# Optimization experiments

Measured on AMD Instinct MI355X. Metric: run time of the kernel, lower is better.

Reference implementation:

```python
import jax, jax.numpy as jnp
import numpy as np

B, V, P, D = 32, 6, 197, 512
L = 77          # CLIP token length
C = 5           # num quality perspectives (conditions)

def _normalize(x, axis=-1, eps=1e-12):
    n = jnp.linalg.norm(x, axis=axis, keepdims=True)
    return x / jnp.maximum(n, eps)

def _conv3x3(x, w, b):
    # x: [C,112,7,7], w: [O,112,3,3] -> [C,O,7,7]
    y = jax.lax.conv_general_dilated(x, w, (1, 1), 'SAME',
                                     dimension_numbers=('NCHW', 'OIHW', 'NCHW'))
    return y + b[None, :, None, None]

def setup_inputs() -> dict:
    key = jax.random.key(0)
    ks = jax.random.split(key, 20)
    s = 0.02  # weight init scale keeps sigmoids in linear-ish range
    return {
        'feature_texture': jax.random.normal(ks[0], (B, V * P, D), jnp.float32),
        'feature_prompt': jax.random.normal(ks[1], (B, L, D), jnp.float32),
        'feature_prompt_eot': jax.random.normal(ks[2], (B, D), jnp.float32),
        'feature_condition': jax.random.normal(ks[3], (C, D), jnp.float32),
        'fc_quality_w': jax.random.normal(ks[4], (224, D), jnp.float32) * s,
        'fc_quality_b': jnp.zeros((224,), jnp.float32),
        'fc_condition_w': jax.random.normal(ks[5], (5488, D), jnp.float32) * s,
        'fc_condition_b': jnp.zeros((5488,), jnp.float32),
        'fc1w_conv_w': jax.random.normal(ks[6], (512, 112, 3, 3), jnp.float32) * s,
        'fc1w_conv_b': jnp.zeros((512,), jnp.float32),
        'fc2w_conv_w': jax.random.normal(ks[7], (128, 112, 3, 3), jnp.float32) * s,
        'fc2w_conv_b': jnp.zeros((128,), jnp.float32),
        'fc3w_conv_w': jax.random.normal(ks[8], (32, 112, 3, 3), jnp.float32) * s,
        'fc3w_conv_b': jnp.zeros((32,), jnp.float32),
        'fc4w_conv_w': jax.random.normal(ks[9], (8, 112, 3, 3), jnp.float32) * s,
        'fc4w_conv_b': jnp.zeros((8,), jnp.float32),
        'fc1b_w': jax.random.normal(ks[10], (112, 112), jnp.float32) * s,
        'fc1b_b': jnp.zeros((112,), jnp.float32),
        'fc2b_w': jax.random.normal(ks[11], (56, 112), jnp.float32) * s,
        'fc2b_b': jnp.zeros((56,), jnp.float32),
        'fc3b_w': jax.random.normal(ks[12], (28, 112), jnp.float32) * s,
        'fc3b_b': jnp.zeros((28,), jnp.float32),
        'fc4b_w': jax.random.normal(ks[13], (14, 112), jnp.float32) * s,
        'fc4b_b': jnp.zeros((14,), jnp.float32),
        'fc5w_w': jax.random.normal(ks[14], (14, 112), jnp.float32) * s,
        'fc5w_b': jnp.zeros((14,), jnp.float32),
        'fc5b_w': jax.random.normal(ks[15], (1, 112), jnp.float32) * s,
        'fc5b_b': jnp.zeros((1,), jnp.float32),
    }

def reference(feature_texture, feature_prompt, feature_prompt_eot, feature_condition,
              fc_quality_w, fc_quality_b, fc_condition_w, fc_condition_b,
              fc1w_conv_w, fc1w_conv_b, fc2w_conv_w, fc2w_conv_b,
              fc3w_conv_w, fc3w_conv_b, fc4w_conv_w, fc4w_conv_b,
              fc1b_w, fc1b_b, fc2b_w, fc2b_b, fc3b_w, fc3b_b, fc4b_w, fc4b_b,
              fc5w_w, fc5w_b, fc5b_w, fc5b_b):
    nC = feature_condition.shape[0]

    # --- calculate_cos: mean of relu(pairwise cosine sim), upper triangle i<j ---
    fn = _normalize(feature_condition)                      # [C,512]
    gram = fn @ fn.T                                        # [C,C]
    iu, ju = jnp.triu_indices(nC, k=1)
    loss_dis = jnp.mean(jnp.maximum(gram[iu, ju], 0.0))

    # --- cross-attention-style patch weighting ---
    np_prompt = _normalize(feature_prompt, axis=2)          # [B,L,D]
    np_tex = _normalize(feature_texture, axis=2)            # [B,J,D]
    sim_texture = jnp.einsum('bid,bjd->bji', np_prompt, np_tex)   # [B,J,L]
    sim_cond = jnp.einsum('bid,cd->bci', np_prompt, fn)           # [B,C,L]
    patch_weight = jnp.einsum('bcl,bjl->bjc', sim_cond, sim_texture)  # [B,J,C]
    patch_weight = jax.nn.softmax(patch_weight, axis=1)

    # --- condition feature maps for hypernet: [C,112,7,7] ---
    cond_maps = (feature_condition @ fc_condition_w.T + fc_condition_b)
    cond_maps = cond_maps.reshape(nC, 112, 7, 7)

    # --- hypernet: generate TargetNet params for all conditions at once ---
    pooled = cond_maps.mean(axis=(2, 3))                              # [C,112]
    fc1w = _conv3x3(cond_maps, fc1w_conv_w, fc1w_conv_b).reshape(nC, 112, 224)
    fc2w = _conv3x3(cond_maps, fc2w_conv_w, fc2w_conv_b).reshape(nC, 56, 112)
    fc3w = _conv3x3(cond_maps, fc3w_conv_w, fc3w_conv_b).reshape(nC, 28, 56)
    fc4w = _conv3x3(cond_maps, fc4w_conv_w, fc4w_conv_b).reshape(nC, 14, 28)
    fc1b = pooled @ fc1b_w.T + fc1b_b                                 # [C,112]
    fc2b = pooled @ fc2b_w.T + fc2b_b                                 # [C,56]
    fc3b = pooled @ fc3b_w.T + fc3b_b                                 # [C,28]
    fc4b = pooled @ fc4b_w.T + fc4b_b                                 # [C,14]
    fc5w = pooled @ fc5w_w.T + fc5w_b                                 # [C,14]
    fc5b = pooled @ fc5b_w.T + fc5b_b                                 # [C,1]

    # --- fused quality feature per (batch, condition) ---
    ftf = jnp.einsum('bjd,bjc->bcd', feature_texture, patch_weight)   # [B,C,D]
    fused = ftf * feature_prompt_eot[:, None, :]                      # [B,C,D]
    fq = jnp.einsum('bcd,kd->bck', fused, fc_quality_w) + fc_quality_b  # [B,C,224]

    # --- TargetNet (per-condition generated weights), vectorized over loop ---
    h = jax.nn.sigmoid(jnp.einsum('bck,cjk->bcj', fq, fc1w) + fc1b[None])
    h = jax.nn.sigmoid(jnp.einsum('bcj,cij->bci', h, fc2w) + fc2b[None])
    h = jax.nn.sigmoid(jnp.einsum('bci,coi->bco', h, fc3w) + fc3b[None])
    h = jax.nn.sigmoid(jnp.einsum('bco,cpo->bcp', h, fc4w) + fc4b[None])
    score_list = jnp.einsum('bcp,cp->bc', h, fc5w) + fc5b[:, 0][None]  # [B,C]

    return score_list, loss_dis
```

## Files before the change

### kernel.cpp

```cpp
#include <hip/hip_runtime.h>
#include <hip/hip_bf16.h>
#include <math.h>

#define B_   32
#define J_   1182
#define D_   512
#define L_   77
#define C_   5
#define JC_  64
#define NCH_ 19
#define NPW_ 37

__device__ __forceinline__ float dot4(float4 a, float4 b) {
    return a.x*b.x + a.y*b.y + a.z*b.z + a.w*b.w;
}

__device__ __forceinline__ float wave_sum(float v) {
#pragma unroll
    for (int off = 32; off > 0; off >>= 1) v += __shfl_xor(v, off, 64);
    return v;
}

__device__ __forceinline__ float wave_max(float v) {
#pragma unroll
    for (int off = 32; off > 0; off >>= 1) v = fmaxf(v, __shfl_xor(v, off, 64));
    return v;
}

__global__ void k_front(const float* __restrict__ fc, const float* __restrict__ cw,
                        const float* __restrict__ cb, float* __restrict__ cm,
                        float* __restrict__ loss_out,
                        const float* __restrict__ fp, float* __restrict__ swl) {
    __shared__ float4 smem4[640];
    float* sfc = (float*)smem4;
    int bid = blockIdx.x, t = threadIdx.x;
    int wave = t >> 6, lane = t & 63;

    if (bid < 1373) {
        for (int i = t; i < C_*D_; i += 256) sfc[i] = fc[i];
        __syncthreads();

        if (bid == 1372) {
            for (int c = wave; c < C_; c += 4) {
                float ss = 0.f;
                for (int d = lane; d < D_; d += 64) { float v = sfc[c*D_+d]; ss += v*v; }
                ss = wave_sum(ss);
                float inv = 1.f / fmaxf(sqrtf(ss), 1e-12f);
                for (int d = lane; d < D_; d += 64) sfc[c*D_+d] *= inv;
            }
            __syncthreads();
            if (wave == 0) {
                float acc = 0.f;
                for (int i = 0; i < C_; ++i)
                    for (int j = i+1; j < C_; ++j) {
                        float p = 0.f;
                        for (int d = lane; d < D_; d += 64) p += sfc[i*D_+d]*sfc[j*D_+d];
                        p = wave_sum(p);
                        acc += fmaxf(p, 0.f);
                    }
                if (lane == 0) *loss_out = acc * (1.f/10.f);
            }
            return;
        }

        int o = bid*4 + wave;
        const float4* w4 = (const float4*)(cw + (size_t)o*D_);
        float4 wa = w4[lane], wb = w4[lane+64];
        float bias = cb[o];
        float keep = 0.f;
#pragma unroll
        for (int c = 0; c < C_; ++c) {
            const float4* f4 = (const float4*)(sfc + c*D_);
            float s = dot4(wa, f4[lane]) + dot4(wb, f4[lane+64]);
            s = wave_sum(s);
            if (lane == c) keep = s;
        }
        if (lane < C_) cm[lane*5488 + o] = keep + bias;
        return;
    }

    for (int c = wave; c < C_; c += 4) {
        const float4* f8 = (const float4*)(fc + c*D_);
        float4 v0 = f8[lane*2], v1 = f8[lane*2+1];
        float ss = dot4(v0,v0) + dot4(v1,v1);
        ss = wave_sum(ss);
        float inv = 1.f / fmaxf(sqrtf(ss), 1e-12f);
        v0.x*=inv; v0.y*=inv; v0.z*=inv; v0.w*=inv;
        v1.x*=inv; v1.y*=inv; v1.z*=inv; v1.w*=inv;
        int f0 = lane*2, f1 = lane*2+1;
        smem4[(c*16 + (f0 & 15))*8 + (f0 >> 4)] = v0;
        smem4[(c*16 + (f1 & 15))*8 + (f1 >> 4)] = v1;
    }
    __syncthreads();

    int row = t >> 3, seg = t & 7;
    int bl = (bid - 1373)*32 + row;
    int b = bl / L_, l = bl - b*L_;
    const float4* p4 = ((const float4*)(fp + (size_t)bl*D_)) + seg*16;
    float ss=0.f, s0=0.f, s1=0.f, s2=0.f, s3=0.f, s4=0.f;
#pragma unroll 4
    for (int k = 0; k < 16; ++k) {
        float4 v = p4[k];
        int base = k*8 + seg;
        ss += dot4(v, v);
        s0 += dot4(v, smem4[base]);
        s1 += dot4(v, smem4[128 + base]);
        s2 += dot4(v, smem4[256 + base]);
        s3 += dot4(v, smem4[384 + base]);
        s4 += dot4(v, smem4[512 + base]);
    }
#pragma unroll
    for (int off = 1; off < 8; off <<= 1) {
        ss += __shfl_xor(ss,off,64);
        s0 += __shfl_xor(s0,off,64); s1 += __shfl_xor(s1,off,64);
        s2 += __shfl_xor(s2,off,64); s3 += __shfl_xor(s3,off,64);
        s4 += __shfl_xor(s4,off,64);
    }
    if (seg == 0) {
        float inv = 1.f / fmaxf(sqrtf(ss), 1e-12f);
        float inv2 = inv*inv;
        swl[((size_t)(b*C_+0))*L_ + l] = s0*inv2;
        swl[((size_t)(b*C_+1))*L_ + l] = s1*inv2;
        swl[((size_t)(b*C_+2))*L_ + l] = s2*inv2;
        swl[((size_t)(b*C_+3))*L_ + l] = s3*inv2;
        swl[((size_t)(b*C_+4))*L_ + l] = s4*inv2;
    }
}

__global__ void k_Q(const float* __restrict__ fp, const float* __restrict__ swl,
                    float* __restrict__ Q) {
    __shared__ float sw[C_][80];
    int b = blockIdx.y;
    int t = threadIdx.x;
    for (int i = t; i < C_*L_; i += 256) { int c = i/L_, l = i - c*L_; sw[c][l] = swl[((size_t)(b*C_+c))*L_ + l]; }
    __syncthreads();
    int d = blockIdx.x*256 + t;
    float a0=0.f, a1=0.f, a2=0.f, a3=0.f, a4=0.f;
    const float* f = fp + (size_t)b*L_*D_ + d;
    for (int l = 0; l < L_; ++l) {
        float v = f[(size_t)l*D_];
        a0 += sw[0][l]*v; a1 += sw[1][l]*v; a2 += sw[2][l]*v;
        a3 += sw[3][l]*v; a4 += sw[4][l]*v;
    }
    Q[(size_t)(b*C_+0)*D_ + d] = a0;
    Q[(size_t)(b*C_+1)*D_ + d] = a1;
    Q[(size_t)(b*C_+2)*D_ + d] = a2;
    Q[(size_t)(b*C_+3)*D_ + d] = a3;
    Q[(size_t)(b*C_+4)*D_ + d] = a4;
}

__global__ void k_conv_pw(const float* __restrict__ cm,
                          const float* __restrict__ w1, const float* __restrict__ bb1,
                          const float* __restrict__ w2, const float* __restrict__ bb2,
                          const float* __restrict__ w3, const float* __restrict__ bb3,
                          const float* __restrict__ w4, const float* __restrict__ bb4,
                          float* __restrict__ o1, float* __restrict__ o2,
                          float* __restrict__ o3, float* __restrict__ o4,
                          const float* __restrict__ w1b, const float* __restrict__ b1b,
                          const float* __restrict__ w2b, const float* __restrict__ b2b,
                          const float* __restrict__ w3b, const float* __restrict__ b3b,
                          const float* __restrict__ w4b, const float* __restrict__ b4b,
                          const float* __restrict__ w5w, const float* __restrict__ b5w,
                          const float* __restrict__ w5b, const float* __restrict__ b5b,
                          float* __restrict__ fcb,
                          const float* __restrict__ tex, const float* __restrict__ Q,
                          float* __restrict__ pw, float2* __restrict__ pstat) {
    __shared__ float4 smem4[3052];
    __shared__ float sp[112];
    int bid = blockIdx.x;
    int t = threadIdx.x;
    bool is_conv = (bid < 1500) && ((bid & 3) == 0);

    if (!is_conv) {
        int p = (bid >= 1500) ? (bid - 375) : (bid - 1 - (bid >> 2));
        float4* qs = smem4;
        float* sraw = (float*)(smem4 + 640);
        int bx = p % NPW_, b = p / NPW_;
        {
            const float4* q4 = (const float4*)(Q + (size_t)b*C_*D_);
            for (int i = t; i < C_*128; i += 256) {
                int c = i >> 7, f = i & 127;
                qs[(c*16 + (f & 15))*8 + (f >> 4)] = q4[i];
            }
        }
        __syncthreads();
        int row = t >> 3, seg = t & 7;
        int j = bx*32 + row;
        bool valid = (j < J_);
        int jc = valid ? j : (J_-1);
        const float4* tp = (const float4*)(tex + ((size_t)(b*J_ + jc))*D_ + seg*64);
        float ss=0.f, s0=0.f, s1=0.f, s2=0.f, s3=0.f, s4=0.f;
#pragma unroll 4
        for (int k = 0; k < 16; ++k) {
            float4 v = tp[k];
            int base = k*8 + seg;
            ss += dot4(v, v);
            s0 += dot4(v, qs[base]);
            s1 += dot4(v, qs[128 + base]);
            s2 += dot4(v, qs[256 + base]);
            s3 += dot4(v, qs[384 + base]);
            s4 += dot4(v, qs[512 + base]);
        }
#pragma unroll
        for (int off = 1; off < 8; off <<= 1) {
            ss += __shfl_xor(ss,off,64);
            s0 += __shfl_xor(s0,off,64); s1 += __shfl_xor(s1,off,64);
            s2 += __shfl_xor(s2,off,64); s3 += __shfl_xor(s3,off,64);
            s4 += __shfl_xor(s4,off,64);
        }
        if (seg == 0) {
            float inv = 1.f / fmaxf(sqrtf(ss), 1e-12f);
            float r0 = s0*inv, r1 = s1*inv, r2 = s2*inv, r3 = s3*inv, r4 = s4*inv;
            if (valid) {
                pw[((size_t)(b*C_+0))*J_ + j] = r0;
                pw[((size_t)(b*C_+1))*J_ + j] = r1;
                pw[((size_t)(b*C_+2))*J_ + j] = r2;
                pw[((size_t)(b*C_+3))*J_ + j] = r3;
                pw[((size_t)(b*C_+4))*J_ + j] = r4;
                sraw[0*32+row]=r0; sraw[1*32+row]=r1; sraw[2*32+row]=r2;
                sraw[3*32+row]=r3; sraw[4*32+row]=r4;
            } else {
                sraw[0*32+row]=-1e30f; sraw[1*32+row]=-1e30f; sraw[2*32+row]=-1e30f;
                sraw[3*32+row]=-1e30f; sraw[4*32+row]=-1e30f;
            }
        }
        __syncthreads();
        if (t < C_*32) {
            int c = t >> 5, r2 = t & 31;
            float v = sraw[c*32 + r2];
            float m = v;
#pragma unroll
            for (int off = 1; off < 32; off <<= 1) m = fmaxf(m, __shfl_xor(m,off,32));
            float e = (v > -1e29f) ? expf(v - m) : 0.f;
#pragma unroll
            for (int off = 1; off < 32; off <<= 1) e += __shfl_xor(e,off,32);
            if (r2 == 0) pstat[(size_t)(bx*B_ + b)*C_ + c] = make_float2(m, e);
        }
        return;
    }

    int conv_id = bid >> 2;
    float* im = (float*)smem4;
    int c  = conv_id / 75;
    int bx = conv_id - c*75;
    for (int i = t; i < 112*108; i += 256) im[i] = 0.f;
    __syncthreads();
    const float* cmc = cm + c*5488;
    for (int i = t; i < 112*49; i += 256) {
        int ch = i / 49, yx = i - ch*49;
        int y = yx / 7, x = yx - y*7;
        im[ch*108 + (y+1)*12 + (x+1)] = cmc[i];
    }
    __syncthreads();

    if (bx == 0) {
        if (t < 112) {
            const float* p = im + t*108;
            float s = 0.f;
            for (int k = 0; k < 108; ++k) s += p[k];
            sp[t] = s * (1.f/49.f);
        }
        __syncthreads();
        if (t < 225) {
            int rel = t;
            const float* w; const float* bb; int nout; int base;
            if      (rel < 112) {            w=w1b; bb=b1b; nout=112; base=0; }
            else if (rel < 168) { rel-=112;  w=w2b; bb=b2b; nout=56;  base=560; }
            else if (rel < 196) { rel-=168;  w=w3b; bb=b3b; nout=28;  base=840; }
            else if (rel < 210) { rel-=196;  w=w4b; bb=b4b; nout=14;  base=980; }
            else if (rel < 224) { rel-=210;  w=w5w; bb=b5w; nout=14;  base=1050; }
            else                { rel-=224;  w=w5b; bb=b5b; nout=1;   base=1120; }
            float s = bb[rel];
            const float* wr = w + rel*112;
            for (int i = 0; i < 112; ++i) s += sp[i]*wr[i];
            fcb[base + c*nout + rel] = s;
        }
    }

    int oyl = t & 63;
    int chq = t >> 6;
    int oy  = bx*64 + oyl;
    bool ovalid = (oy < 4760);
    int oyc = ovalid ? oy : 0;
    int o_comb = oyc / 7, y = oyc - o_comb*7;
    const float* w; int o;
    if      (o_comb < 512) { w=w1; o=o_comb; }
    else if (o_comb < 640) { w=w2; o=o_comb-512; }
    else if (o_comb < 672) { w=w3; o=o_comb-640; }
    else                   { w=w4; o=o_comb-672; }

    float ac0=0,ac1=0,ac2=0,ac3=0,ac4=0,ac5=0,ac6=0;
    const float* wbase = w + ((size_t)o*112 + chq*28)*9;
    const float* imc   = im + (chq*28)*108 + y*12;
#pragma unroll 2
    for (int ch = 0; ch < 28; ++ch) {
        const float* wk = wbase + ch*9;
        const float* ii = imc + ch*108;
        float w0=wk[0],w1_=wk[1],w2_=wk[2],w3_=wk[3],w4_=wk[4],w5_=wk[5],w6_=wk[6],w7_=wk[7],w8_=wk[8];
#pragma unroll
        for (int ky = 0; ky < 3; ++ky) {
            const float* row = ii + ky*12;
            float4 ra = *(const float4*)(row);
            float4 rb = *(const float4*)(row + 4);
            float  rc = row[8];
            float r0=ra.x,r1=ra.y,r2=ra.z,r3=ra.w,r4=rb.x,r5=rb.y,r6=rb.z,r7=rb.w,r8=rc;
            float wk0 = (ky==0)?w0:((ky==1)?w3_:w6_);
            float wk1 = (ky==0)?w1_:((ky==1)?w4_:w7_);
            float wk2 = (ky==0)?w2_:((ky==1)?w5_:w8_);
            ac0 += r0*wk0 + r1*wk1 + r2*wk2;
            ac1 += r1*wk0 + r2*wk1 + r3*wk2;
            ac2 += r2*wk0 + r3*wk1 + r4*wk2;
            ac3 += r3*wk0 + r4*wk1 + r5*wk2;
            ac4 += r4*wk0 + r5*wk1 + r6*wk2;
            ac5 += r5*wk0 + r6*wk1 + r7*wk2;
            ac6 += r6*wk0 + r7*wk1 + r8*wk2;
        }
    }
    __syncthreads();
    float* partb = im;
    {
        int pb = (chq*64 + oyl)*9;
        partb[pb+0]=ac0; partb[pb+1]=ac1; partb[pb+2]=ac2; partb[pb+3]=ac3;
        partb[pb+4]=ac4; partb[pb+5]=ac5; partb[pb+6]=ac6;
    }
    __syncthreads();
    for (int i = t; i < 448; i += 256) {
        int oyl2 = i / 7, x = i - oyl2*7;
        int oy2 = bx*64 + oyl2;
        if (oy2 < 4760) {
            float s = partb[(0*64+oyl2)*9+x] + partb[(1*64+oyl2)*9+x]
                    + partb[(2*64+oyl2)*9+x] + partb[(3*64+oyl2)*9+x];
            int oc = oy2/7, yy = oy2 - oc*7;
            const float* bias; float* outp; int oo;
            if      (oc < 512) { bias=bb1; outp=o1 + (size_t)c*512*49; oo=oc; }
            else if (oc < 640) { bias=bb2; outp=o2 + (size_t)c*128*49; oo=oc-512; }
            else if (oc < 672) { bias=bb3; outp=o3 + (size_t)c*32*49;  oo=oc-640; }
            else               { bias=bb4; outp=o4 + (size_t)c*8*49;   oo=oc-672; }
            outp[oo*49 + yy*7 + x] = s + bias[oo];
        }
    }
}

__global__ void k_ftf(const float* __restrict__ tex, const float* __restrict__ pwraw,
                      const float2* __restrict__ pstat, float* __restrict__ part) {
    __shared__ float sw[C_][JC_];
    __shared__ float2 sL[C_];
    int chunk = blockIdx.x, b = blockIdx.y;
    int t = threadIdx.x;
    int wave = t >> 6, lane = t & 63;
    if (wave < C_) {
        float2 pv = (lane < NPW_) ? pstat[(size_t)(lane*B_ + b)*C_ + wave]
                                  : make_float2(-1e30f, 0.f);
        float m = wave_max(pv.x);
        float contrib = (lane < NPW_) ? pv.y * expf(pv.x - m) : 0.f;
        float denom = wave_sum(contrib);
        if (lane == 0) sL[wave] = make_float2(m, 1.f/denom);
    }
    __syncthreads();
    int j0 = chunk*JC_;
    int jn = min(JC_, J_ - j0);
    if (t < C_*JC_) {
        int c = t >> 6, jj = t & 63;
        float2 ms = sL[c];
        sw[c][jj] = (jj < jn)
            ? expf(pwraw[((size_t)(b*C_+c))*J_ + j0 + jj] - ms.x) * ms.y
            : 0.f;
    }
    __syncthreads();
    float acc0=0.f, acc1=0.f, acc2=0.f, acc3=0.f, acc4=0.f;
    const float* tp = tex + ((size_t)b*J_ + j0)*D_ + t;
    for (int jj = 0; jj < jn; ++jj) {
        float v = tp[(size_t)jj*D_];
        acc0 += v*sw[0][jj]; acc1 += v*sw[1][jj]; acc2 += v*sw[2][jj];
        acc3 += v*sw[3][jj]; acc4 += v*sw[4][jj];
    }
    size_t base = (((size_t)chunk*B_ + b)*C_)*D_ + t;
    part[base               ] = acc0;
    part[base +   (size_t)D_] = acc1;
    part[base + 2*(size_t)D_] = acc2;
    part[base + 3*(size_t)D_] = acc3;
    part[base + 4*(size_t)D_] = acc4;
}

__global__ void k_fq_target(const float* __restrict__ part, const float* __restrict__ eot,
                            const float* __restrict__ qw, const float* __restrict__ qb,
                            const float* __restrict__ g1w, const float* __restrict__ g2w,
                            const float* __restrict__ g3w, const float* __restrict__ g4w,
                            const float* __restrict__ fcb, float* __restrict__ out) {
    int bc = blockIdx.x; int b = bc / C_; int c = bc - b*C_;
    __shared__ float sf[D_];
    __shared__ float sa[224], sb[112];
    int t = threadIdx.x;

    float s0 = 0.f, s1 = 0.f;
    for (int ch = 0; ch < NCH_; ++ch) {
        const float* p = part + ((size_t)ch*(B_*C_) + bc)*D_;
        s0 += p[t]; s1 += p[t+256];
    }
    sf[t]     = s0 * eot[b*D_ + t];
    sf[t+256] = s1 * eot[b*D_ + t + 256];
    __syncthreads();

    if (t < 224) {
        const float4* w4 = (const float4*)(qw + (size_t)t*D_);
        const float4* s4 = (const float4*)sf;
        float acc = 0.f;
#pragma unroll 4
        for (int i = 0; i < 128; ++i) acc += dot4(s4[i], w4[i]);
        sa[t] = acc + qb[t];
    }
    __syncthreads();

    if (t < 112) {
        const float* w = g1w + (size_t)c*25088 + t*224;
        float s = fcb[c*112 + t];
        for (int k = 0; k < 224; ++k) s += w[k]*sa[k];
        sb[t] = 1.f/(1.f+expf(-s));
    }
    __syncthreads();
    if (t < 56) {
        const float* w = g2w + (size_t)c*6272 + t*112;
        float s = fcb[560 + c*56 + t];
        for (int k = 0; k < 112; ++k) s += w[k]*sb[k];
        sa[t] = 1.f/(1.f+expf(-s));
    }
    __syncthreads();
    if (t < 28) {
        const float* w = g3w + (size_t)c*1568 + t*56;
        float s = fcb[840 + c*28 + t];
        for (int k = 0; k < 56; ++k) s += w[k]*sa[k];
        sb[t] = 1.f/(1.f+expf(-s));
    }
    __syncthreads();
    if (t < 14) {
        const float* w = g4w + (size_t)c*392 + t*28;
        float s = fcb[980 + c*14 + t];
        for (int k = 0; k < 28; ++k) s += w[k]*sb[k];
        sa[t] = 1.f/(1.f+expf(-s));
    }
    __syncthreads();
    if (t == 0) {
        float s = fcb[1120 + c];
        for (int p = 0; p < 14; ++p) s += sa[p]*fcb[1050 + c*14 + p];
        out[b*C_ + c] = s;
    }
}

extern "C" void kernel_launch(void* const* d_in, const int* in_sizes, int n_in,
                              void* d_out, int out_size, void* d_ws, size_t ws_size,
                              hipStream_t stream) {
    (void)in_sizes; (void)n_in; (void)out_size; (void)ws_size;
    const float* tex   = (const float*)d_in[0];
    const float* fp    = (const float*)d_in[1];
    const float* eot   = (const float*)d_in[2];
    const float* fcond = (const float*)d_in[3];
    const float* qw    = (const float*)d_in[4];
    const float* qb    = (const float*)d_in[5];
    const float* cw    = (const float*)d_in[6];
    const float* cb    = (const float*)d_in[7];
    const float* w1c   = (const float*)d_in[8];  const float* b1c = (const float*)d_in[9];
    const float* w2c   = (const float*)d_in[10]; const float* b2c = (const float*)d_in[11];
    const float* w3c   = (const float*)d_in[12]; const float* b3c = (const float*)d_in[13];
    const float* w4c   = (const float*)d_in[14]; const float* b4c = (const float*)d_in[15];
    const float* f1bw  = (const float*)d_in[16]; const float* f1bb = (const float*)d_in[17];
    const float* f2bw  = (const float*)d_in[18]; const float* f2bb = (const float*)d_in[19];
    const float* f3bw  = (const float*)d_in[20]; const float* f3bb = (const float*)d_in[21];
    const float* f4bw  = (const float*)d_in[22]; const float* f4bb = (const float*)d_in[23];
    const float* f5ww  = (const float*)d_in[24]; const float* f5wb = (const float*)d_in[25];
    const float* f5bw  = (const float*)d_in[26]; const float* f5bb = (const float*)d_in[27];
    float* out = (float*)d_out;

    float* ws     = (float*)d_ws;
    float* Qb     = ws;
    float* pw     = Qb + 81920;
    float* part   = pw + 189120;
    float* pstat  = part + 1556480;
    float* cm     = pstat + 11840;
    float* g1w    = cm + 27440;
    float* g2w    = g1w + 125440;
    float* g3w    = g2w + 31360;
    float* g4w    = g3w + 7840;
    float* fcb    = g4w + 1960;
    float* swl    = fcb + 1125;

    k_front<<<1450, 256, 0, stream>>>(fcond, cw, cb, cm, out + B_*C_, fp, swl);
    k_Q<<<dim3(2, B_), 256, 0, stream>>>(fp, swl, Qb);
    k_conv_pw<<<1559, 256, 0, stream>>>(cm, w1c, b1c, w2c, b2c, w3c, b3c, w4c, b4c,
                                        g1w, g2w, g3w, g4w,
                                        f1bw, f1bb, f2bw, f2bb, f3bw, f3bb,
                                        f4bw, f4bb, f5ww, f5wb, f5bw, f5bb, fcb,
                                        tex, Qb, pw, (float2*)pstat);
    k_ftf<<<dim3(NCH_, B_), 512, 0, stream>>>(tex, pw, (const float2*)pstat, part);
    k_fq_target<<<B_*C_, 256, 0, stream>>>(part, eot, qw, qb,
                                           g1w, g2w, g3w, g4w, fcb, out);
}
```

Before: 101.7 us.

## Stage texture rows in padded LDS and shrink patch-weight tiles to 16 rows

The patch-weight part of the fused conv kernel now loads 16 texture rows per block with coalesced float4 reads into padded shared memory, then computes norms and query dot products from LDS with 16 lanes per row. Previously each block handled 32 rows read directly from global memory. The conv blocks are no longer interleaved with the patch-weight blocks; they occupy the first 375 block IDs. Doubling the number of patch-weight tiles doubles the partial softmax stats, so the k_ftf reduction reads two stats per lane and the workspace offsets are shifted. This adds occupancy pressure from roughly 48KB of LDS per block in exchange for better load coalescing and more parallelism.

```diff
diff --git a/kernel.cpp b/kernel.cpp
--- a/kernel.cpp
+++ b/kernel.cpp
@@ -9,7 +9,8 @@
 #define C_   5
 #define JC_  64
 #define NCH_ 19
-#define NPW_ 37
+#define NPW_ 74
+#define JPW_ 16
 
 __device__ __forceinline__ float dot4(float4 a, float4 b) {
     return a.x*b.x + a.y*b.y + a.z*b.z + a.w*b.w;
@@ -165,84 +166,103 @@
                           float* __restrict__ fcb,
                           const float* __restrict__ tex, const float* __restrict__ Q,
                           float* __restrict__ pw, float2* __restrict__ pstat) {
-    __shared__ float4 smem4[3052];
-    __shared__ float sp[112];
+    __shared__ float smem[12352];
     int bid = blockIdx.x;
     int t = threadIdx.x;
-    bool is_conv = (bid < 1500) && ((bid & 3) == 0);
-
-    if (!is_conv) {
-        int p = (bid >= 1500) ? (bid - 375) : (bid - 1 - (bid >> 2));
-        float4* qs = smem4;
-        float* sraw = (float*)(smem4 + 640);
+
+    if (bid >= 375) {
+        float* stex = smem;
+        float* sq   = smem + 9216;
+        float* srawT = smem + 12096;
+        int p = bid - 375;
         int bx = p % NPW_, b = p / NPW_;
+        int j0 = bx*JPW_;
+        int jn = min(JPW_, J_ - j0);
+
         {
             const float4* q4 = (const float4*)(Q + (size_t)b*C_*D_);
             for (int i = t; i < C_*128; i += 256) {
-                int c = i >> 7, f = i & 127;
-                qs[(c*16 + (f & 15))*8 + (f >> 4)] = q4[i];
+                int c = i >> 7, col4 = i & 127;
+                *(float4*)(sq + c*576 + col4*4 + ((col4>>3)<<2)) = q4[i];
+            }
+            const float4* t4 = (const float4*)(tex + ((size_t)(b*J_ + j0))*D_);
+#pragma unroll
+            for (int n = 0; n < 8; ++n) {
+                int i = n*256 + t;
+                int row = i >> 7, col4 = i & 127;
+                if (row < jn)
+                    *(float4*)(stex + row*576 + col4*4 + ((col4>>3)<<2)) = t4[i];
             }
         }
         __syncthreads();
-        int row = t >> 3, seg = t & 7;
-        int j = bx*32 + row;
-        bool valid = (j < J_);
-        int jc = valid ? j : (J_-1);
-        const float4* tp = (const float4*)(tex + ((size_t)(b*J_ + jc))*D_ + seg*64);
-        float ss=0.f, s0=0.f, s1=0.f, s2=0.f, s3=0.f, s4=0.f;
-#pragma unroll 4
-        for (int k = 0; k < 16; ++k) {
-            float4 v = tp[k];
-            int base = k*8 + seg;
-            ss += dot4(v, v);
-            s0 += dot4(v, qs[base]);
-            s1 += dot4(v, qs[128 + base]);
-            s2 += dot4(v, qs[256 + base]);
-            s3 += dot4(v, qs[384 + base]);
-            s4 += dot4(v, qs[512 + base]);
-        }
-#pragma unroll
-        for (int off = 1; off < 8; off <<= 1) {
-            ss += __shfl_xor(ss,off,64);
-            s0 += __shfl_xor(s0,off,64); s1 += __shfl_xor(s1,off,64);
-            s2 += __shfl_xor(s2,off,64); s3 += __shfl_xor(s3,off,64);
-            s4 += __shfl_xor(s4,off,64);
-        }
-        if (seg == 0) {
-            float inv = 1.f / fmaxf(sqrtf(ss), 1e-12f);
-            float r0 = s0*inv, r1 = s1*inv, r2 = s2*inv, r3 = s3*inv, r4 = s4*inv;
-            if (valid) {
-                pw[((size_t)(b*C_+0))*J_ + j] = r0;
-                pw[((size_t)(b*C_+1))*J_ + j] = r1;
-                pw[((size_t)(b*C_+2))*J_ + j] = r2;
-                pw[((size_t)(b*C_+3))*J_ + j] = r3;
-                pw[((size_t)(b*C_+4))*J_ + j] = r4;
-                sraw[0*32+row]=r0; sraw[1*32+row]=r1; sraw[2*32+row]=r2;
-                sraw[3*32+row]=r3; sraw[4*32+row]=r4;
-            } else {
-                sraw[0*32+row]=-1e30f; sraw[1*32+row]=-1e30f; sraw[2*32+row]=-1e30f;
-                sraw[3*32+row]=-1e30f; sraw[4*32+row]=-1e30f;
+
+        {
+            int row = t >> 4, seg = t & 15;
+            const float* sr = stex + row*576;
+            float ss=0.f, s0=0.f, s1=0.f, s2=0.f, s3=0.f, s4=0.f;
+#pragma unroll
+            for (int k = 0; k < 8; ++k) {
+                int col4 = seg*8 + k;
+                int wa = col4*4 + ((col4>>3)<<2);
+                float4 v = *(const float4*)(sr + wa);
+                ss += dot4(v, v);
+                s0 += dot4(v, *(const float4*)(sq +          wa));
+                s1 += dot4(v, *(const float4*)(sq +   576 + wa));
+                s2 += dot4(v, *(const float4*)(sq + 2*576 + wa));
+                s3 += dot4(v, *(const float4*)(sq + 3*576 + wa));
+                s4 += dot4(v, *(const float4*)(sq + 4*576 + wa));
+            }
+#pragma unroll
+            for (int off = 1; off < 16; off <<= 1) {
+                ss += __shfl_xor(ss,off,64);
+                s0 += __shfl_xor(s0,off,64); s1 += __shfl_xor(s1,off,64);
+                s2 += __shfl_xor(s2,off,64); s3 += __shfl_xor(s3,off,64);
+                s4 += __shfl_xor(s4,off,64);
+            }
+            if (seg == 0) {
+                if (row < jn) {
+                    float inv = 1.f / fmaxf(sqrtf(ss), 1e-12f);
+                    float r0=s0*inv, r1=s1*inv, r2=s2*inv, r3=s3*inv, r4=s4*inv;
+                    int j = j0 + row;
+                    pw[((size_t)(b*C_+0))*J_ + j] = r0;
+                    pw[((size_t)(b*C_+1))*J_ + j] = r1;
+                    pw[((size_t)(b*C_+2))*J_ + j] = r2;
+                    pw[((size_t)(b*C_+3))*J_ + j] = r3;
+                    pw[((size_t)(b*C_+4))*J_ + j] = r4;
+                    srawT[row*8+0]=r0; srawT[row*8+1]=r1; srawT[row*8+2]=r2;
+                    srawT[row*8+3]=r3; srawT[row*8+4]=r4;
+                } else {
+                    srawT[row*8+0]=-1e30f; srawT[row*8+1]=-1e30f; srawT[row*8+2]=-1e30f;
+                    srawT[row*8+3]=-1e30f; srawT[row*8+4]=-1e30f;
+                }
             }
         }
         __syncthreads();
-        if (t < C_*32) {
-            int c = t >> 5, r2 = t & 31;
-            float v = sraw[c*32 + r2];
-            float m = v;
-#pragma unroll
-            for (int off = 1; off < 32; off <<= 1) m = fmaxf(m, __shfl_xor(m,off,32));
-            float e = (v > -1e29f) ? expf(v - m) : 0.f;
-#pragma unroll
-            for (int off = 1; off < 32; off <<= 1) e += __shfl_xor(e,off,32);
-            if (r2 == 0) pstat[(size_t)(bx*B_ + b)*C_ + c] = make_float2(m, e);
+
+        {
+            int wave = t >> 6, lane = t & 63;
+            bool act = (wave == 0) || (wave == 1 && lane < 16);
+            if (act) {
+                int c = (wave == 0) ? (lane >> 4) : 4;
+                int row = lane & 15;
+                float v = srawT[row*8+c];
+                float m = v;
+#pragma unroll
+                for (int off = 1; off < 16; off <<= 1) m = fmaxf(m, __shfl_xor(m,off,64));
+                float e = (row < jn) ? expf(v - m) : 0.f;
+                float s = e;
+#pragma unroll
+                for (int off = 1; off < 16; off <<= 1) s += __shfl_xor(s,off,64);
+                if (row == 0) pstat[(size_t)(bx*B_+b)*C_ + c] = make_float2(m, s);
+            }
         }
         return;
     }
 
-    int conv_id = bid >> 2;
-    float* im = (float*)smem4;
-    int c  = conv_id / 75;
-    int bx = conv_id - c*75;
+    float* im = smem;
+    float* sp = smem + 12096;
+    int c  = bid / 75;
+    int bx = bid - c*75;
     for (int i = t; i < 112*108; i += 256) im[i] = 0.f;
     __syncthreads();
     const float* cmc = cm + c*5488;
@@ -280,8 +300,7 @@
     int oyl = t & 63;
     int chq = t >> 6;
     int oy  = bx*64 + oyl;
-    bool ovalid = (oy < 4760);
-    int oyc = ovalid ? oy : 0;
+    int oyc = (oy < 4760) ? oy : 0;
     int o_comb = oyc / 7, y = oyc - o_comb*7;
     const float* w; int o;
     if      (o_comb < 512) { w=w1; o=o_comb; }
@@ -349,10 +368,12 @@
     int t = threadIdx.x;
     int wave = t >> 6, lane = t & 63;
     if (wave < C_) {
-        float2 pv = (lane < NPW_) ? pstat[(size_t)(lane*B_ + b)*C_ + wave]
+        float2 pa = (lane < NPW_) ? pstat[(size_t)(lane*B_ + b)*C_ + wave]
                                   : make_float2(-1e30f, 0.f);
-        float m = wave_max(pv.x);
-        float contrib = (lane < NPW_) ? pv.y * expf(pv.x - m) : 0.f;
+        float2 pb = (lane+64 < NPW_) ? pstat[(size_t)((lane+64)*B_ + b)*C_ + wave]
+                                     : make_float2(-1e30f, 0.f);
+        float m = wave_max(fmaxf(pa.x, pb.x));
+        float contrib = pa.y * expf(pa.x - m) + pb.y * expf(pb.x - m);
         float denom = wave_sum(contrib);
         if (lane == 0) sL[wave] = make_float2(m, 1.f/denom);
     }
@@ -475,7 +496,7 @@
     float* pw     = Qb + 81920;
     float* part   = pw + 189120;
     float* pstat  = part + 1556480;
-    float* cm     = pstat + 11840;
+    float* cm     = pstat + 23680;
     float* g1w    = cm + 27440;
     float* g2w    = g1w + 125440;
     float* g3w    = g2w + 31360;
@@ -485,7 +506,7 @@
 
     k_front<<<1450, 256, 0, stream>>>(fcond, cw, cb, cm, out + B_*C_, fp, swl);
     k_Q<<<dim3(2, B_), 256, 0, stream>>>(fp, swl, Qb);
-    k_conv_pw<<<1559, 256, 0, stream>>>(cm, w1c, b1c, w2c, b2c, w3c, b3c, w4c, b4c,
+    k_conv_pw<<<375 + NPW_*B_, 256, 0, stream>>>(cm, w1c, b1c, w2c, b2c, w3c, b3c, w4c, b4c,
                                         g1w, g2w, g3w, g4w,
                                         f1bw, f1bb, f2bw, f2bb, f3bw, f3bb,
                                         f4bw, f4bb, f5ww, f5wb, f5bw, f5bb, fcb,
```

New measurement: 90.54 us. 1.12x faster.
